# Performance work log

Hardware: AMD Instinct MI355X
Metric: run time of the kernel (lower is better)

The kernel has to match this reference:

```python
import jax, jax.numpy as jnp
import numpy as np

N_NODES = 10000
N_EDGES = 640000
D_IN = 128
D_OUT = 128


def setup_inputs() -> dict:
    key = jax.random.key(0)
    k_x, k_src, k_dst, k_w, k_b = jax.random.split(key, 5)
    x = jax.random.normal(k_x, (N_NODES, D_IN), dtype=jnp.float32)
    src = jax.random.randint(k_src, (N_EDGES,), 0, N_NODES, dtype=jnp.int64)
    dst = jax.random.randint(k_dst, (N_EDGES,), 0, N_NODES, dtype=jnp.int64)
    # nn.Linear default init: U(-1/sqrt(fan_in), 1/sqrt(fan_in))
    bound = 1.0 / np.sqrt(D_IN)
    W = jax.random.uniform(k_w, (D_OUT, D_IN), minval=-bound, maxval=bound, dtype=jnp.float32)
    b = jax.random.uniform(k_b, (D_OUT,), minval=-bound, maxval=bound, dtype=jnp.float32)
    return {"x": x, "src": src, "dst": dst, "W": W, "b": b}


def reference(x, src, dst, W, b):
    # Message passing: gather source-node features per edge, scatter-sum to dst.
    msg = x[src]  # [E, D_IN]
    h = jax.ops.segment_sum(msg, dst, num_segments=N_NODES)  # [N, D_IN]
    # Dense linear: h @ W.T + b
    return jnp.einsum("nd,od->no", h, W) + b
```

## Files before the change

kernel.cpp:

```cpp
#include <hip/hip_runtime.h>
#include <hip/hip_bf16.h>
#include <stdint.h>


#define NBLK 128
#define CBSH 4
#define CBSZ 16
#define NCMAX 640
#define CAP 44
#define CAPN 192

typedef __attribute__((ext_vector_type(8))) short bf16x8;
typedef __attribute__((ext_vector_type(4))) float f32x4;

static __device__ inline unsigned short f2bf(float f) {
    unsigned int u = __float_as_uint(f);
    u += 0x7fffu + ((u >> 16) & 1u);
    return (unsigned short)(u >> 16);
}

__global__ __launch_bounds__(512) void k_fused(const float* __restrict__ x,
                                               const float* __restrict__ W,
                                               unsigned short* __restrict__ y,
                                               int N, int xwb,
                                               const void* __restrict__ srcv,
                                               const void* __restrict__ dstv,
                                               unsigned int* __restrict__ staging,
                                               unsigned short* __restrict__ cnts,
                                               int NC, int E, int C) {
    __shared__ uint4 shbuf[2048];
    __shared__ unsigned int shAny;
    int t = threadIdx.x;
    if ((int)blockIdx.x < NBLK) {
        int* cur = (int*)shbuf;
        if (t == 0) shAny = 0u;
        __syncthreads();
        if (t < 256) {
            unsigned int v = ((const unsigned int*)srcv)[2 * t + 1];
            if (v) atomicOr(&shAny, 1u);
        }
        int bid = blockIdx.x;
        for (int i = t; i < NC; i += 512) cur[i] = (bid * NC + i) * CAP;
        __syncthreads();
        int f64 = shAny ? 0 : 1;
        int beg = bid * C, end = min(E, beg + C);
        int nfull = (end - beg) & ~3;
        if (f64) {
            const long long* s = (const long long*)srcv;
            const long long* d = (const long long*)dstv;
            for (int e0 = beg + 4 * t; e0 < beg + nfull; e0 += 4 * 512) {
                ulonglong2 dA = *(const ulonglong2*)(d + e0);
                ulonglong2 dB = *(const ulonglong2*)(d + e0 + 2);
                ulonglong2 sA = *(const ulonglong2*)(s + e0);
                ulonglong2 sB = *(const ulonglong2*)(s + e0 + 2);
                int dv[4] = {(int)dA.x, (int)dA.y, (int)dB.x, (int)dB.y};
                int sv[4] = {(int)sA.x, (int)sA.y, (int)sB.x, (int)sB.y};
#pragma unroll
                for (int j = 0; j < 4; ++j) {
                    int cb = dv[j] >> CBSH;
                    int pos = atomicAdd(&cur[cb], 1);
                    if (pos - (bid * NC + cb) * CAP < CAP)
                        staging[pos] = ((unsigned int)(dv[j] & (CBSZ - 1)) << 16) |
                                       (unsigned int)sv[j];
                }
            }
            int te = beg + nfull + t;
            if (te < end) {
                int dv = (int)d[te];
                int cb = dv >> CBSH;
                int pos = atomicAdd(&cur[cb], 1);
                if (pos - (bid * NC + cb) * CAP < CAP)
                    staging[pos] = ((unsigned int)(dv & (CBSZ - 1)) << 16) |
                                   (unsigned int)(int)s[te];
            }
        } else {
            const int* s = (const int*)srcv;
            const int* d = (const int*)dstv;
            for (int e0 = beg + 4 * t; e0 < beg + nfull; e0 += 4 * 512) {
                uint4 d4 = *(const uint4*)(d + e0);
                uint4 s4 = *(const uint4*)(s + e0);
                int dv[4] = {(int)d4.x, (int)d4.y, (int)d4.z, (int)d4.w};
                int sv[4] = {(int)s4.x, (int)s4.y, (int)s4.z, (int)s4.w};
#pragma unroll
                for (int j = 0; j < 4; ++j) {
                    int cb = dv[j] >> CBSH;
                    int pos = atomicAdd(&cur[cb], 1);
                    if (pos - (bid * NC + cb) * CAP < CAP)
                        staging[pos] = ((unsigned int)(dv[j] & (CBSZ - 1)) << 16) |
                                       (unsigned int)sv[j];
                }
            }
            int te = beg + nfull + t;
            if (te < end) {
                int dv = d[te];
                int cb = dv >> CBSH;
                int pos = atomicAdd(&cur[cb], 1);
                if (pos - (bid * NC + cb) * CAP < CAP)
                    staging[pos] = ((unsigned int)(dv & (CBSZ - 1)) << 16) |
                                   (unsigned int)s[te];
            }
        }
        __syncthreads();
        for (int i = t; i < NC; i += 512) {
            int cnt = cur[i] - (bid * NC + i) * CAP;
            if (cnt > CAP) cnt = CAP;
            cnts[(size_t)i * NBLK + bid] = (unsigned short)cnt;
        }
    } else {
        for (int i = t; i < 2048; i += 512) {
            int o = i >> 4, g = i & 15;
            const float4* wp = (const float4*)(W + o * 128 + g * 8);
            float4 f0 = wp[0], f1 = wp[1];
            uint4 pk;
            pk.x = (unsigned int)f2bf(f0.x) | ((unsigned int)f2bf(f0.y) << 16);
            pk.y = (unsigned int)f2bf(f0.z) | ((unsigned int)f2bf(f0.w) << 16);
            pk.z = (unsigned int)f2bf(f1.x) | ((unsigned int)f2bf(f1.y) << 16);
            pk.w = (unsigned int)f2bf(f1.z) | ((unsigned int)f2bf(f1.w) << 16);
            shbuf[o * 16 + (g ^ (o & 15))] = pk;
        }
        __syncthreads();
        int wid = (blockIdx.x - NBLK) * 8 + (t >> 6);
        int lane = t & 63;
        int m0 = wid * 16;
        if (m0 >= N) return;
        int r = lane & 15, hi = lane >> 4;
        int mr = m0 + r; if (mr >= N) mr = N - 1;
        bf16x8 a[4];
        const float* xr = x + (size_t)mr * 128 + hi * 8;
#pragma unroll
        for (int kt = 0; kt < 4; ++kt) {
            float4 f0 = *(const float4*)(xr + kt * 32);
            float4 f1 = *(const float4*)(xr + kt * 32 + 4);
            unsigned short* ap = (unsigned short*)&a[kt];
            ap[0]=f2bf(f0.x); ap[1]=f2bf(f0.y); ap[2]=f2bf(f0.z); ap[3]=f2bf(f0.w);
            ap[4]=f2bf(f1.x); ap[5]=f2bf(f1.y); ap[6]=f2bf(f1.z); ap[7]=f2bf(f1.w);
        }
#pragma unroll 2
        for (int ot = 0; ot < 8; ++ot) {
            f32x4 acc = {0.f, 0.f, 0.f, 0.f};
            int o = ot * 16 + r;
#pragma unroll
            for (int kt = 0; kt < 4; ++kt) {
                uint4 wv4 = shbuf[o * 16 + ((kt * 4 + hi) ^ (o & 15))];
                bf16x8 bf;
                *(uint4*)&bf = wv4;
                acc = __builtin_amdgcn_mfma_f32_16x16x32_bf16(a[kt], bf, acc, 0, 0, 0);
            }
#pragma unroll
            for (int reg = 0; reg < 4; ++reg) {
                int m = m0 + hi * 4 + reg;
                if (m < N) y[(size_t)m * 128 + ot * 16 + r] = f2bf(acc[reg]);
            }
        }
    }
}

__global__ __launch_bounds__(512) void k_sortgather(const unsigned int* __restrict__ staging,
                                                    const unsigned short* __restrict__ cnts,
                                                    const unsigned short* __restrict__ y,
                                                    const float* __restrict__ bias,
                                                    float* __restrict__ out,
                                                    int N, int NC) {
    __shared__ unsigned short sorted[CBSZ * CAPN];
    __shared__ int wcnt[NBLK];
    __shared__ int nodeCnt[CBSZ];
    int c = blockIdx.x, t = threadIdx.x;
    if (t < 64) {
        unsigned int pv = ((const unsigned int*)(cnts + (size_t)c * NBLK))[t];
        wcnt[2 * t] = (int)(pv & 0xFFFFu);
        wcnt[2 * t + 1] = (int)(pv >> 16);
    }
    if (t >= 64 && t < 64 + CBSZ) nodeCnt[t - 64] = 0;
    __syncthreads();
    int gq = t >> 3, ln8 = t & 7;
#pragma unroll
    for (int i = 0; i < 2; ++i) {
        int k = gq + i * 64;
        int cw = wcnt[k];
        const unsigned int* srcw = staging + ((size_t)k * NC + c) * CAP;
        for (int j = ln8; j < cw; j += 8) {
            unsigned int p = srcw[j];
            int node = (int)(p >> 16);
            int pos = atomicAdd(&nodeCnt[node], 1);
            if (pos < CAPN)
                sorted[node * CAPN + pos] = (unsigned short)(p & 0xFFFFu);
        }
    }
    __syncthreads();
    int wv = t >> 6, lane = t & 63;
    int r = lane & 15, g = lane >> 4;
    const uint4* yp = (const uint4*)y;
#pragma unroll
    for (int q = 0; q < 2; ++q) {
        int tloc = wv * 2 + q;
        int node = (c << CBSH) + tloc;
        if (node >= N) continue;
        int lcnt = nodeCnt[tloc]; if (lcnt > CAPN) lcnt = CAPN;
        const unsigned short* sl = sorted + tloc * CAPN;
        float2 a0 = {0.f,0.f}, a1 = {0.f,0.f}, a2 = {0.f,0.f}, a3 = {0.f,0.f};
        int nb4 = lcnt >> 2;
#pragma unroll 4
        for (int k = 0; k < nb4; ++k) {
            int sid = (int)sl[4 * k + g];
            uint4 v = yp[(size_t)sid * 16 + r];
            a0.x += __uint_as_float(v.x << 16); a0.y += __uint_as_float(v.x & 0xffff0000u);
            a1.x += __uint_as_float(v.y << 16); a1.y += __uint_as_float(v.y & 0xffff0000u);
            a2.x += __uint_as_float(v.z << 16); a2.y += __uint_as_float(v.z & 0xffff0000u);
            a3.x += __uint_as_float(v.w << 16); a3.y += __uint_as_float(v.w & 0xffff0000u);
        }
        int idx = (nb4 << 2) + g;
        if (idx < lcnt) {
            int sid = (int)sl[idx];
            uint4 v = yp[(size_t)sid * 16 + r];
            a0.x += __uint_as_float(v.x << 16); a0.y += __uint_as_float(v.x & 0xffff0000u);
            a1.x += __uint_as_float(v.y << 16); a1.y += __uint_as_float(v.y & 0xffff0000u);
            a2.x += __uint_as_float(v.z << 16); a2.y += __uint_as_float(v.z & 0xffff0000u);
            a3.x += __uint_as_float(v.w << 16); a3.y += __uint_as_float(v.w & 0xffff0000u);
        }
        a0.x += __shfl_xor(a0.x, 16); a0.x += __shfl_xor(a0.x, 32);
        a0.y += __shfl_xor(a0.y, 16); a0.y += __shfl_xor(a0.y, 32);
        a1.x += __shfl_xor(a1.x, 16); a1.x += __shfl_xor(a1.x, 32);
        a1.y += __shfl_xor(a1.y, 16); a1.y += __shfl_xor(a1.y, 32);
        a2.x += __shfl_xor(a2.x, 16); a2.x += __shfl_xor(a2.x, 32);
        a2.y += __shfl_xor(a2.y, 16); a2.y += __shfl_xor(a2.y, 32);
        a3.x += __shfl_xor(a3.x, 16); a3.x += __shfl_xor(a3.x, 32);
        a3.y += __shfl_xor(a3.y, 16); a3.y += __shfl_xor(a3.y, 32);
        if (lane < 16) {
            float4 b0 = ((const float4*)bias)[r * 2];
            float4 b1 = ((const float4*)bias)[r * 2 + 1];
            float4 o0 = {a0.x + b0.x, a0.y + b0.y, a1.x + b0.z, a1.y + b0.w};
            float4 o1 = {a2.x + b1.x, a2.y + b1.y, a3.x + b1.z, a3.y + b1.w};
            float4* op = (float4*)(out + (size_t)node * 128 + r * 8);
            op[0] = o0;
            op[1] = o1;
        }
    }
}

extern "C" void kernel_launch(void* const* d_in, const int* in_sizes, int n_in,
                              void* d_out, int out_size, void* d_ws, size_t ws_size,
                              hipStream_t stream) {
    const float* x = (const float*)d_in[0];
    const void* srcv = d_in[1];
    const void* dstv = d_in[2];
    const float* W = (const float*)d_in[3];
    const float* bias = (const float*)d_in[4];
    float* out = (float*)d_out;

    const int D = 128;
    int N = in_sizes[0] / D;
    int E = in_sizes[1];
    int C = (E + NBLK - 1) / NBLK;
    int NC = (N + CBSZ - 1) >> CBSH;

    char* ws = (char*)d_ws;
    size_t off = 0;
    auto take = [&](size_t bytes) {
        char* p = ws + off;
        off = (off + bytes + 255) & ~(size_t)255;
        return p;
    };
    unsigned short* y      = (unsigned short*)take((size_t)N * D * 2);
    unsigned int* staging  = (unsigned int*)take((size_t)NBLK * NC * CAP * 4);
    unsigned short* cnts   = (unsigned short*)take((size_t)NC * NBLK * 2);

    int xwb = (((N + 15) / 16) + 7) / 8;

    k_fused<<<NBLK + xwb, 512, 0, stream>>>(x, W, y, N, xwb, srcv, dstv,
                                            staging, cnts, NC, E, C);
    k_sortgather<<<NC, 512, 0, stream>>>(staging, cnts, y, bias, out, N, NC);
}
```

Measured before the change: 29.80 us.

## Double binning blocks and block size, interleave two-node gather loops

Binning now uses 256 blocks of 1024 threads, so each block handles half as many edges, and the per-bucket staging capacity drops from 44 to 24 slots. The GEMM part also runs 1024-thread blocks. In the sort-gather kernel, each wave interleaves the gather loops for its two nodes so more independent loads are in flight, and the count load is widened to four entries per thread. The smaller capacity makes bucket overflow, which silently drops edges, more likely for skewed inputs, and the 1024-thread blocks may reduce occupancy.

```diff
diff --git a/kernel.cpp b/kernel.cpp
--- a/kernel.cpp
+++ b/kernel.cpp
@@ -3,11 +3,11 @@
 #include <stdint.h>
 
 
-#define NBLK 128
+#define NBLK 256
 #define CBSH 4
 #define CBSZ 16
 #define NCMAX 640
-#define CAP 44
+#define CAP 24
 #define CAPN 192
 
 typedef __attribute__((ext_vector_type(8))) short bf16x8;
@@ -19,15 +19,15 @@
     return (unsigned short)(u >> 16);
 }
 
-__global__ __launch_bounds__(512) void k_fused(const float* __restrict__ x,
-                                               const float* __restrict__ W,
-                                               unsigned short* __restrict__ y,
-                                               int N, int xwb,
-                                               const void* __restrict__ srcv,
-                                               const void* __restrict__ dstv,
-                                               unsigned int* __restrict__ staging,
-                                               unsigned short* __restrict__ cnts,
-                                               int NC, int E, int C) {
+__global__ __launch_bounds__(1024) void k_fused(const float* __restrict__ x,
+                                                const float* __restrict__ W,
+                                                unsigned short* __restrict__ y,
+                                                int N, int xwb,
+                                                const void* __restrict__ srcv,
+                                                const void* __restrict__ dstv,
+                                                unsigned int* __restrict__ staging,
+                                                unsigned short* __restrict__ cnts,
+                                                int NC, int E, int C) {
     __shared__ uint4 shbuf[2048];
     __shared__ unsigned int shAny;
     int t = threadIdx.x;
@@ -40,7 +40,7 @@
             if (v) atomicOr(&shAny, 1u);
         }
         int bid = blockIdx.x;
-        for (int i = t; i < NC; i += 512) cur[i] = (bid * NC + i) * CAP;
+        for (int i = t; i < NC; i += 1024) cur[i] = (bid * NC + i) * CAP;
         __syncthreads();
         int f64 = shAny ? 0 : 1;
         int beg = bid * C, end = min(E, beg + C);
@@ -48,7 +48,7 @@
         if (f64) {
             const long long* s = (const long long*)srcv;
             const long long* d = (const long long*)dstv;
-            for (int e0 = beg + 4 * t; e0 < beg + nfull; e0 += 4 * 512) {
+            for (int e0 = beg + 4 * t; e0 < beg + nfull; e0 += 4 * 1024) {
                 ulonglong2 dA = *(const ulonglong2*)(d + e0);
                 ulonglong2 dB = *(const ulonglong2*)(d + e0 + 2);
                 ulonglong2 sA = *(const ulonglong2*)(s + e0);
@@ -76,7 +76,7 @@
         } else {
             const int* s = (const int*)srcv;
             const int* d = (const int*)dstv;
-            for (int e0 = beg + 4 * t; e0 < beg + nfull; e0 += 4 * 512) {
+            for (int e0 = beg + 4 * t; e0 < beg + nfull; e0 += 4 * 1024) {
                 uint4 d4 = *(const uint4*)(d + e0);
                 uint4 s4 = *(const uint4*)(s + e0);
                 int dv[4] = {(int)d4.x, (int)d4.y, (int)d4.z, (int)d4.w};
@@ -101,13 +101,13 @@
             }
         }
         __syncthreads();
-        for (int i = t; i < NC; i += 512) {
+        for (int i = t; i < NC; i += 1024) {
             int cnt = cur[i] - (bid * NC + i) * CAP;
             if (cnt > CAP) cnt = CAP;
             cnts[(size_t)i * NBLK + bid] = (unsigned short)cnt;
         }
     } else {
-        for (int i = t; i < 2048; i += 512) {
+        for (int i = t; i < 2048; i += 1024) {
             int o = i >> 4, g = i & 15;
             const float4* wp = (const float4*)(W + o * 128 + g * 8);
             float4 f0 = wp[0], f1 = wp[1];
@@ -119,7 +119,7 @@
             shbuf[o * 16 + (g ^ (o & 15))] = pk;
         }
         __syncthreads();
-        int wid = (blockIdx.x - NBLK) * 8 + (t >> 6);
+        int wid = (blockIdx.x - NBLK) * 16 + (t >> 6);
         int lane = t & 63;
         int m0 = wid * 16;
         if (m0 >= N) return;
@@ -166,15 +166,17 @@
     __shared__ int nodeCnt[CBSZ];
     int c = blockIdx.x, t = threadIdx.x;
     if (t < 64) {
-        unsigned int pv = ((const unsigned int*)(cnts + (size_t)c * NBLK))[t];
-        wcnt[2 * t] = (int)(pv & 0xFFFFu);
-        wcnt[2 * t + 1] = (int)(pv >> 16);
+        uint2 pv = ((const uint2*)(cnts + (size_t)c * NBLK))[t];
+        wcnt[4*t]   = (int)(pv.x & 0xFFFFu);
+        wcnt[4*t+1] = (int)(pv.x >> 16);
+        wcnt[4*t+2] = (int)(pv.y & 0xFFFFu);
+        wcnt[4*t+3] = (int)(pv.y >> 16);
     }
     if (t >= 64 && t < 64 + CBSZ) nodeCnt[t - 64] = 0;
     __syncthreads();
     int gq = t >> 3, ln8 = t & 7;
 #pragma unroll
-    for (int i = 0; i < 2; ++i) {
+    for (int i = 0; i < 4; ++i) {
         int k = gq + i * 64;
         int cw = wcnt[k];
         const unsigned int* srcw = staging + ((size_t)k * NC + c) * CAP;
@@ -190,49 +192,76 @@
     int wv = t >> 6, lane = t & 63;
     int r = lane & 15, g = lane >> 4;
     const uint4* yp = (const uint4*)y;
-#pragma unroll
-    for (int q = 0; q < 2; ++q) {
-        int tloc = wv * 2 + q;
-        int node = (c << CBSH) + tloc;
-        if (node >= N) continue;
-        int lcnt = nodeCnt[tloc]; if (lcnt > CAPN) lcnt = CAPN;
-        const unsigned short* sl = sorted + tloc * CAPN;
-        float2 a0 = {0.f,0.f}, a1 = {0.f,0.f}, a2 = {0.f,0.f}, a3 = {0.f,0.f};
-        int nb4 = lcnt >> 2;
-#pragma unroll 4
-        for (int k = 0; k < nb4; ++k) {
-            int sid = (int)sl[4 * k + g];
+    int tloc0 = wv * 2, tloc1 = wv * 2 + 1;
+    int node0 = (c << CBSH) + tloc0, node1 = node0 + 1;
+    int lc0 = nodeCnt[tloc0]; if (lc0 > CAPN) lc0 = CAPN;
+    int lc1 = nodeCnt[tloc1]; if (lc1 > CAPN) lc1 = CAPN;
+    const unsigned short* sl0 = sorted + tloc0 * CAPN;
+    const unsigned short* sl1 = sorted + tloc1 * CAPN;
+    float2 p0[4] = {{0.f,0.f},{0.f,0.f},{0.f,0.f},{0.f,0.f}};
+    float2 p1[4] = {{0.f,0.f},{0.f,0.f},{0.f,0.f},{0.f,0.f}};
+    int nb0 = lc0 >> 2, nb1 = lc1 >> 2;
+    int nbmax = nb0 > nb1 ? nb0 : nb1;
+#pragma unroll 2
+    for (int k = 0; k < nbmax; ++k) {
+        if (k < nb0) {
+            int sid = (int)sl0[4 * k + g];
             uint4 v = yp[(size_t)sid * 16 + r];
-            a0.x += __uint_as_float(v.x << 16); a0.y += __uint_as_float(v.x & 0xffff0000u);
-            a1.x += __uint_as_float(v.y << 16); a1.y += __uint_as_float(v.y & 0xffff0000u);
-            a2.x += __uint_as_float(v.z << 16); a2.y += __uint_as_float(v.z & 0xffff0000u);
-            a3.x += __uint_as_float(v.w << 16); a3.y += __uint_as_float(v.w & 0xffff0000u);
-        }
-        int idx = (nb4 << 2) + g;
-        if (idx < lcnt) {
-            int sid = (int)sl[idx];
+            p0[0].x += __uint_as_float(v.x << 16); p0[0].y += __uint_as_float(v.x & 0xffff0000u);
+            p0[1].x += __uint_as_float(v.y << 16); p0[1].y += __uint_as_float(v.y & 0xffff0000u);
+            p0[2].x += __uint_as_float(v.z << 16); p0[2].y += __uint_as_float(v.z & 0xffff0000u);
+            p0[3].x += __uint_as_float(v.w << 16); p0[3].y += __uint_as_float(v.w & 0xffff0000u);
+        }
+        if (k < nb1) {
+            int sid = (int)sl1[4 * k + g];
             uint4 v = yp[(size_t)sid * 16 + r];
-            a0.x += __uint_as_float(v.x << 16); a0.y += __uint_as_float(v.x & 0xffff0000u);
-            a1.x += __uint_as_float(v.y << 16); a1.y += __uint_as_float(v.y & 0xffff0000u);
-            a2.x += __uint_as_float(v.z << 16); a2.y += __uint_as_float(v.z & 0xffff0000u);
-            a3.x += __uint_as_float(v.w << 16); a3.y += __uint_as_float(v.w & 0xffff0000u);
-        }
-        a0.x += __shfl_xor(a0.x, 16); a0.x += __shfl_xor(a0.x, 32);
-        a0.y += __shfl_xor(a0.y, 16); a0.y += __shfl_xor(a0.y, 32);
-        a1.x += __shfl_xor(a1.x, 16); a1.x += __shfl_xor(a1.x, 32);
-        a1.y += __shfl_xor(a1.y, 16); a1.y += __shfl_xor(a1.y, 32);
-        a2.x += __shfl_xor(a2.x, 16); a2.x += __shfl_xor(a2.x, 32);
-        a2.y += __shfl_xor(a2.y, 16); a2.y += __shfl_xor(a2.y, 32);
-        a3.x += __shfl_xor(a3.x, 16); a3.x += __shfl_xor(a3.x, 32);
-        a3.y += __shfl_xor(a3.y, 16); a3.y += __shfl_xor(a3.y, 32);
-        if (lane < 16) {
-            float4 b0 = ((const float4*)bias)[r * 2];
-            float4 b1 = ((const float4*)bias)[r * 2 + 1];
-            float4 o0 = {a0.x + b0.x, a0.y + b0.y, a1.x + b0.z, a1.y + b0.w};
-            float4 o1 = {a2.x + b1.x, a2.y + b1.y, a3.x + b1.z, a3.y + b1.w};
-            float4* op = (float4*)(out + (size_t)node * 128 + r * 8);
-            op[0] = o0;
-            op[1] = o1;
+            p1[0].x += __uint_as_float(v.x << 16); p1[0].y += __uint_as_float(v.x & 0xffff0000u);
+            p1[1].x += __uint_as_float(v.y << 16); p1[1].y += __uint_as_float(v.y & 0xffff0000u);
+            p1[2].x += __uint_as_float(v.z << 16); p1[2].y += __uint_as_float(v.z & 0xffff0000u);
+            p1[3].x += __uint_as_float(v.w << 16); p1[3].y += __uint_as_float(v.w & 0xffff0000u);
+        }
+    }
+    {
+        int idx = (nb0 << 2) + g;
+        if (idx < lc0) {
+            int sid = (int)sl0[idx];
+            uint4 v = yp[(size_t)sid * 16 + r];
+            p0[0].x += __uint_as_float(v.x << 16); p0[0].y += __uint_as_float(v.x & 0xffff0000u);
+            p0[1].x += __uint_as_float(v.y << 16); p0[1].y += __uint_as_float(v.y & 0xffff0000u);
+            p0[2].x += __uint_as_float(v.z << 16); p0[2].y += __uint_as_float(v.z & 0xffff0000u);
+            p0[3].x += __uint_as_float(v.w << 16); p0[3].y += __uint_as_float(v.w & 0xffff0000u);
+        }
+        idx = (nb1 << 2) + g;
+        if (idx < lc1) {
+            int sid = (int)sl1[idx];
+            uint4 v = yp[(size_t)sid * 16 + r];
+            p1[0].x += __uint_as_float(v.x << 16); p1[0].y += __uint_as_float(v.x & 0xffff0000u);
+            p1[1].x += __uint_as_float(v.y << 16); p1[1].y += __uint_as_float(v.y & 0xffff0000u);
+            p1[2].x += __uint_as_float(v.z << 16); p1[2].y += __uint_as_float(v.z & 0xffff0000u);
+            p1[3].x += __uint_as_float(v.w << 16); p1[3].y += __uint_as_float(v.w & 0xffff0000u);
+        }
+    }
+#pragma unroll
+    for (int j = 0; j < 4; ++j) {
+        p0[j].x += __shfl_xor(p0[j].x, 16); p0[j].x += __shfl_xor(p0[j].x, 32);
+        p0[j].y += __shfl_xor(p0[j].y, 16); p0[j].y += __shfl_xor(p0[j].y, 32);
+        p1[j].x += __shfl_xor(p1[j].x, 16); p1[j].x += __shfl_xor(p1[j].x, 32);
+        p1[j].y += __shfl_xor(p1[j].y, 16); p1[j].y += __shfl_xor(p1[j].y, 32);
+    }
+    if (lane < 16) {
+        float4 b0 = ((const float4*)bias)[r * 2];
+        float4 b1 = ((const float4*)bias)[r * 2 + 1];
+        if (node0 < N) {
+            float4 o0 = {p0[0].x + b0.x, p0[0].y + b0.y, p0[1].x + b0.z, p0[1].y + b0.w};
+            float4 o1 = {p0[2].x + b1.x, p0[2].y + b1.y, p0[3].x + b1.z, p0[3].y + b1.w};
+            float4* op = (float4*)(out + (size_t)node0 * 128 + r * 8);
+            op[0] = o0; op[1] = o1;
+        }
+        if (node1 < N) {
+            float4 o0 = {p1[0].x + b0.x, p1[0].y + b0.y, p1[1].x + b0.z, p1[1].y + b0.w};
+            float4 o1 = {p1[2].x + b1.x, p1[2].y + b1.y, p1[3].x + b1.z, p1[3].y + b1.w};
+            float4* op = (float4*)(out + (size_t)node1 * 128 + r * 8);
+            op[0] = o0; op[1] = o1;
         }
     }
 }
@@ -264,9 +293,9 @@
     unsigned int* staging  = (unsigned int*)take((size_t)NBLK * NC * CAP * 4);
     unsigned short* cnts   = (unsigned short*)take((size_t)NC * NBLK * 2);
 
-    int xwb = (((N + 15) / 16) + 7) / 8;
-
-    k_fused<<<NBLK + xwb, 512, 0, stream>>>(x, W, y, N, xwb, srcv, dstv,
-                                            staging, cnts, NC, E, C);
+    int xwb = (((N + 15) / 16) + 15) / 16;
+
+    k_fused<<<NBLK + xwb, 1024, 0, stream>>>(x, W, y, N, xwb, srcv, dstv,
+                                             staging, cnts, NC, E, C);
     k_sortgather<<<NC, 512, 0, stream>>>(staging, cnts, y, bias, out, N, NC);
 }
```

Measured after the change: 38.80 us. +30.2%, slower.

## Merge binning, GEMM and gather into one cooperative kernel with grid sync

Applied to the files above, without the earlier changes.

Adds a cooperative kernel that runs the edge-binning and x·W phases, then a grid-wide barrier, then the per-bin sort and gather loop in a grid-stride loop. The two phases share one shared-memory buffer through a union. The goal is to remove the second kernel launch and the gap between the launches. The cost is a grid barrier and a grid capped at 256 or 512 blocks, so some blocks handle more than one of the 625 bins in the gather phase. The old two-kernel path is kept as a fallback when cooperative launch is not available. Each launch also adds host-side device-property and occupancy queries.

```diff
diff --git a/kernel.cpp b/kernel.cpp
--- a/kernel.cpp
+++ b/kernel.cpp
@@ -1,6 +1,9 @@
 #include <hip/hip_runtime.h>
 #include <hip/hip_bf16.h>
+#include <hip/hip_cooperative_groups.h>
 #include <stdint.h>
+
+namespace cg = cooperative_groups;
 
 
 #define NBLK 128
@@ -13,116 +16,121 @@
 typedef __attribute__((ext_vector_type(8))) short bf16x8;
 typedef __attribute__((ext_vector_type(4))) float f32x4;
 
+struct P2Sh {
+    unsigned short sorted[CBSZ * CAPN];
+    int wcnt[NBLK];
+    int nodeCnt[CBSZ];
+};
+union SharedU {
+    uint4 shbuf[2048];
+    P2Sh p2;
+};
+
 static __device__ inline unsigned short f2bf(float f) {
     unsigned int u = __float_as_uint(f);
     u += 0x7fffu + ((u >> 16) & 1u);
     return (unsigned short)(u >> 16);
 }
 
-__global__ __launch_bounds__(512) void k_fused(const float* __restrict__ x,
-                                               const float* __restrict__ W,
-                                               unsigned short* __restrict__ y,
-                                               int N, int xwb,
-                                               const void* __restrict__ srcv,
-                                               const void* __restrict__ dstv,
-                                               unsigned int* __restrict__ staging,
-                                               unsigned short* __restrict__ cnts,
-                                               int NC, int E, int C) {
-    __shared__ uint4 shbuf[2048];
-    __shared__ unsigned int shAny;
-    int t = threadIdx.x;
-    if ((int)blockIdx.x < NBLK) {
-        int* cur = (int*)shbuf;
-        if (t == 0) shAny = 0u;
-        __syncthreads();
-        if (t < 256) {
-            unsigned int v = ((const unsigned int*)srcv)[2 * t + 1];
-            if (v) atomicOr(&shAny, 1u);
-        }
-        int bid = blockIdx.x;
-        for (int i = t; i < NC; i += 512) cur[i] = (bid * NC + i) * CAP;
-        __syncthreads();
-        int f64 = shAny ? 0 : 1;
-        int beg = bid * C, end = min(E, beg + C);
-        int nfull = (end - beg) & ~3;
-        if (f64) {
-            const long long* s = (const long long*)srcv;
-            const long long* d = (const long long*)dstv;
-            for (int e0 = beg + 4 * t; e0 < beg + nfull; e0 += 4 * 512) {
-                ulonglong2 dA = *(const ulonglong2*)(d + e0);
-                ulonglong2 dB = *(const ulonglong2*)(d + e0 + 2);
-                ulonglong2 sA = *(const ulonglong2*)(s + e0);
-                ulonglong2 sB = *(const ulonglong2*)(s + e0 + 2);
-                int dv[4] = {(int)dA.x, (int)dA.y, (int)dB.x, (int)dB.y};
-                int sv[4] = {(int)sA.x, (int)sA.y, (int)sB.x, (int)sB.y};
-#pragma unroll
-                for (int j = 0; j < 4; ++j) {
-                    int cb = dv[j] >> CBSH;
-                    int pos = atomicAdd(&cur[cb], 1);
-                    if (pos - (bid * NC + cb) * CAP < CAP)
-                        staging[pos] = ((unsigned int)(dv[j] & (CBSZ - 1)) << 16) |
-                                       (unsigned int)sv[j];
-                }
-            }
-            int te = beg + nfull + t;
-            if (te < end) {
-                int dv = (int)d[te];
-                int cb = dv >> CBSH;
+static __device__ __forceinline__ void body_passA(
+        int bid, int t, int* cur, unsigned int* shAny,
+        const void* __restrict__ srcv, const void* __restrict__ dstv,
+        unsigned int* __restrict__ staging, unsigned short* __restrict__ cnts,
+        int NC, int E, int C) {
+    if (t == 0) *shAny = 0u;
+    __syncthreads();
+    if (t < 256) {
+        unsigned int v = ((const unsigned int*)srcv)[2 * t + 1];
+        if (v) atomicOr(shAny, 1u);
+    }
+    for (int i = t; i < NC; i += 512) cur[i] = (bid * NC + i) * CAP;
+    __syncthreads();
+    int f64 = *shAny ? 0 : 1;
+    int beg = bid * C, end = min(E, beg + C);
+    int nfull = (end - beg) & ~3;
+    if (f64) {
+        const long long* s = (const long long*)srcv;
+        const long long* d = (const long long*)dstv;
+        for (int e0 = beg + 4 * t; e0 < beg + nfull; e0 += 4 * 512) {
+            ulonglong2 dA = *(const ulonglong2*)(d + e0);
+            ulonglong2 dB = *(const ulonglong2*)(d + e0 + 2);
+            ulonglong2 sA = *(const ulonglong2*)(s + e0);
+            ulonglong2 sB = *(const ulonglong2*)(s + e0 + 2);
+            int dv[4] = {(int)dA.x, (int)dA.y, (int)dB.x, (int)dB.y};
+            int sv[4] = {(int)sA.x, (int)sA.y, (int)sB.x, (int)sB.y};
+#pragma unroll
+            for (int j = 0; j < 4; ++j) {
+                int cb = dv[j] >> CBSH;
                 int pos = atomicAdd(&cur[cb], 1);
                 if (pos - (bid * NC + cb) * CAP < CAP)
-                    staging[pos] = ((unsigned int)(dv & (CBSZ - 1)) << 16) |
-                                   (unsigned int)(int)s[te];
+                    staging[pos] = ((unsigned int)(dv[j] & (CBSZ - 1)) << 16) |
+                                   (unsigned int)sv[j];
             }
-        } else {
-            const int* s = (const int*)srcv;
-            const int* d = (const int*)dstv;
-            for (int e0 = beg + 4 * t; e0 < beg + nfull; e0 += 4 * 512) {
-                uint4 d4 = *(const uint4*)(d + e0);
-                uint4 s4 = *(const uint4*)(s + e0);
-                int dv[4] = {(int)d4.x, (int)d4.y, (int)d4.z, (int)d4.w};
-                int sv[4] = {(int)s4.x, (int)s4.y, (int)s4.z, (int)s4.w};
-#pragma unroll
-                for (int j = 0; j < 4; ++j) {
-                    int cb = dv[j] >> CBSH;
-                    int pos = atomicAdd(&cur[cb], 1);
-                    if (pos - (bid * NC + cb) * CAP < CAP)
-                        staging[pos] = ((unsigned int)(dv[j] & (CBSZ - 1)) << 16) |
-                                       (unsigned int)sv[j];
-                }
-            }
-            int te = beg + nfull + t;
-            if (te < end) {
-                int dv = d[te];
-                int cb = dv >> CBSH;
+        }
+        int te = beg + nfull + t;
+        if (te < end) {
+            int dv = (int)d[te];
+            int cb = dv >> CBSH;
+            int pos = atomicAdd(&cur[cb], 1);
+            if (pos - (bid * NC + cb) * CAP < CAP)
+                staging[pos] = ((unsigned int)(dv & (CBSZ - 1)) << 16) |
+                               (unsigned int)(int)s[te];
+        }
+    } else {
+        const int* s = (const int*)srcv;
+        const int* d = (const int*)dstv;
+        for (int e0 = beg + 4 * t; e0 < beg + nfull; e0 += 4 * 512) {
+            uint4 d4 = *(const uint4*)(d + e0);
+            uint4 s4 = *(const uint4*)(s + e0);
+            int dv[4] = {(int)d4.x, (int)d4.y, (int)d4.z, (int)d4.w};
+            int sv[4] = {(int)s4.x, (int)s4.y, (int)s4.z, (int)s4.w};
+#pragma unroll
+            for (int j = 0; j < 4; ++j) {
+                int cb = dv[j] >> CBSH;
                 int pos = atomicAdd(&cur[cb], 1);
                 if (pos - (bid * NC + cb) * CAP < CAP)
-                    staging[pos] = ((unsigned int)(dv & (CBSZ - 1)) << 16) |
-                                   (unsigned int)s[te];
+                    staging[pos] = ((unsigned int)(dv[j] & (CBSZ - 1)) << 16) |
+                                   (unsigned int)sv[j];
             }
         }
-        __syncthreads();
-        for (int i = t; i < NC; i += 512) {
-            int cnt = cur[i] - (bid * NC + i) * CAP;
-            if (cnt > CAP) cnt = CAP;
-            cnts[(size_t)i * NBLK + bid] = (unsigned short)cnt;
-        }
-    } else {
-        for (int i = t; i < 2048; i += 512) {
-            int o = i >> 4, g = i & 15;
-            const float4* wp = (const float4*)(W + o * 128 + g * 8);
-            float4 f0 = wp[0], f1 = wp[1];
-            uint4 pk;
-            pk.x = (unsigned int)f2bf(f0.x) | ((unsigned int)f2bf(f0.y) << 16);
-            pk.y = (unsigned int)f2bf(f0.z) | ((unsigned int)f2bf(f0.w) << 16);
-            pk.z = (unsigned int)f2bf(f1.x) | ((unsigned int)f2bf(f1.y) << 16);
-            pk.w = (unsigned int)f2bf(f1.z) | ((unsigned int)f2bf(f1.w) << 16);
-            shbuf[o * 16 + (g ^ (o & 15))] = pk;
-        }
-        __syncthreads();
-        int wid = (blockIdx.x - NBLK) * 8 + (t >> 6);
-        int lane = t & 63;
-        int m0 = wid * 16;
-        if (m0 >= N) return;
+        int te = beg + nfull + t;
+        if (te < end) {
+            int dv = d[te];
+            int cb = dv >> CBSH;
+            int pos = atomicAdd(&cur[cb], 1);
+            if (pos - (bid * NC + cb) * CAP < CAP)
+                staging[pos] = ((unsigned int)(dv & (CBSZ - 1)) << 16) |
+                               (unsigned int)s[te];
+        }
+    }
+    __syncthreads();
+    for (int i = t; i < NC; i += 512) {
+        int cnt = cur[i] - (bid * NC + i) * CAP;
+        if (cnt > CAP) cnt = CAP;
+        cnts[(size_t)i * NBLK + bid] = (unsigned short)cnt;
+    }
+}
+
+static __device__ __forceinline__ void body_xw(
+        int blkoff, int t, uint4* shbuf,
+        const float* __restrict__ x, const float* __restrict__ W,
+        unsigned short* __restrict__ y, int N) {
+    for (int i = t; i < 2048; i += 512) {
+        int o = i >> 4, g = i & 15;
+        const float4* wp = (const float4*)(W + o * 128 + g * 8);
+        float4 f0 = wp[0], f1 = wp[1];
+        uint4 pk;
+        pk.x = (unsigned int)f2bf(f0.x) | ((unsigned int)f2bf(f0.y) << 16);
+        pk.y = (unsigned int)f2bf(f0.z) | ((unsigned int)f2bf(f0.w) << 16);
+        pk.z = (unsigned int)f2bf(f1.x) | ((unsigned int)f2bf(f1.y) << 16);
+        pk.w = (unsigned int)f2bf(f1.z) | ((unsigned int)f2bf(f1.w) << 16);
+        shbuf[o * 16 + (g ^ (o & 15))] = pk;
+    }
+    __syncthreads();
+    int wid = blkoff * 8 + (t >> 6);
+    int lane = t & 63;
+    int m0 = wid * 16;
+    if (m0 < N) {
         int r = lane & 15, hi = lane >> 4;
         int mr = m0 + r; if (mr >= N) mr = N - 1;
         bf16x8 a[4];
@@ -155,35 +163,32 @@
     }
 }
 
-__global__ __launch_bounds__(512) void k_sortgather(const unsigned int* __restrict__ staging,
-                                                    const unsigned short* __restrict__ cnts,
-                                                    const unsigned short* __restrict__ y,
-                                                    const float* __restrict__ bias,
-                                                    float* __restrict__ out,
-                                                    int N, int NC) {
-    __shared__ unsigned short sorted[CBSZ * CAPN];
-    __shared__ int wcnt[NBLK];
-    __shared__ int nodeCnt[CBSZ];
-    int c = blockIdx.x, t = threadIdx.x;
+static __device__ __forceinline__ void body_bin(
+        int c, int t, P2Sh* sh,
+        const unsigned int* __restrict__ staging,
+        const unsigned short* __restrict__ cnts,
+        const unsigned short* __restrict__ y,
+        const float* __restrict__ bias, float* __restrict__ out,
+        int N, int NC) {
     if (t < 64) {
         unsigned int pv = ((const unsigned int*)(cnts + (size_t)c * NBLK))[t];
-        wcnt[2 * t] = (int)(pv & 0xFFFFu);
-        wcnt[2 * t + 1] = (int)(pv >> 16);
-    }
-    if (t >= 64 && t < 64 + CBSZ) nodeCnt[t - 64] = 0;
+        sh->wcnt[2 * t] = (int)(pv & 0xFFFFu);
+        sh->wcnt[2 * t + 1] = (int)(pv >> 16);
+    }
+    if (t >= 64 && t < 64 + CBSZ) sh->nodeCnt[t - 64] = 0;
     __syncthreads();
     int gq = t >> 3, ln8 = t & 7;
 #pragma unroll
     for (int i = 0; i < 2; ++i) {
         int k = gq + i * 64;
-        int cw = wcnt[k];
+        int cw = sh->wcnt[k];
         const unsigned int* srcw = staging + ((size_t)k * NC + c) * CAP;
         for (int j = ln8; j < cw; j += 8) {
             unsigned int p = srcw[j];
             int node = (int)(p >> 16);
-            int pos = atomicAdd(&nodeCnt[node], 1);
+            int pos = atomicAdd(&sh->nodeCnt[node], 1);
             if (pos < CAPN)
-                sorted[node * CAPN + pos] = (unsigned short)(p & 0xFFFFu);
+                sh->sorted[node * CAPN + pos] = (unsigned short)(p & 0xFFFFu);
         }
     }
     __syncthreads();
@@ -195,8 +200,8 @@
         int tloc = wv * 2 + q;
         int node = (c << CBSH) + tloc;
         if (node >= N) continue;
-        int lcnt = nodeCnt[tloc]; if (lcnt > CAPN) lcnt = CAPN;
-        const unsigned short* sl = sorted + tloc * CAPN;
+        int lcnt = sh->nodeCnt[tloc]; if (lcnt > CAPN) lcnt = CAPN;
+        const unsigned short* sl = sh->sorted + tloc * CAPN;
         float2 a0 = {0.f,0.f}, a1 = {0.f,0.f}, a2 = {0.f,0.f}, a3 = {0.f,0.f};
         int nb4 = lcnt >> 2;
 #pragma unroll 4
@@ -237,6 +242,58 @@
     }
 }
 
+__global__ __launch_bounds__(512) void k_fused(const float* __restrict__ x,
+                                               const float* __restrict__ W,
+                                               unsigned short* __restrict__ y,
+                                               int N, int xwb,
+                                               const void* __restrict__ srcv,
+                                               const void* __restrict__ dstv,
+                                               unsigned int* __restrict__ staging,
+                                               unsigned short* __restrict__ cnts,
+                                               int NC, int E, int C) {
+    __shared__ uint4 shbuf[2048];
+    __shared__ unsigned int shAny;
+    if ((int)blockIdx.x < NBLK)
+        body_passA(blockIdx.x, threadIdx.x, (int*)shbuf, &shAny,
+                   srcv, dstv, staging, cnts, NC, E, C);
+    else
+        body_xw(blockIdx.x - NBLK, threadIdx.x, shbuf, x, W, y, N);
+}
+
+__global__ __launch_bounds__(512) void k_sortgather(const unsigned int* __restrict__ staging,
+                                                    const unsigned short* __restrict__ cnts,
+                                                    const unsigned short* __restrict__ y,
+                                                    const float* __restrict__ bias,
+                                                    float* __restrict__ out,
+                                                    int N, int NC) {
+    __shared__ P2Sh sh2;
+    body_bin(blockIdx.x, threadIdx.x, &sh2, staging, cnts, y, bias, out, N, NC);
+}
+
+__global__ __launch_bounds__(512) void k_all(
+        const float* __restrict__ x, const float* __restrict__ W,
+        unsigned short* __restrict__ y, int N, int xwb,
+        const void* __restrict__ srcv, const void* __restrict__ dstv,
+        unsigned int* __restrict__ staging, unsigned short* __restrict__ cnts,
+        int NC, int E, int C,
+        const float* __restrict__ bias, float* __restrict__ out) {
+    __shared__ SharedU sh;
+    __shared__ unsigned int shAny;
+    int t = threadIdx.x;
+    if ((int)blockIdx.x < NBLK)
+        body_passA(blockIdx.x, t, (int*)sh.shbuf, &shAny,
+                   srcv, dstv, staging, cnts, NC, E, C);
+    else if ((int)blockIdx.x < NBLK + xwb)
+        body_xw(blockIdx.x - NBLK, t, sh.shbuf, x, W, y, N);
+
+    cg::this_grid().sync();
+
+    for (int c = blockIdx.x; c < NC; c += gridDim.x) {
+        __syncthreads();
+        body_bin(c, t, &sh.p2, staging, cnts, y, bias, out, N, NC);
+    }
+}
+
 extern "C" void kernel_launch(void* const* d_in, const int* in_sizes, int n_in,
                               void* d_out, int out_size, void* d_ws, size_t ws_size,
                               hipStream_t stream) {
@@ -266,7 +323,23 @@
 
     int xwb = (((N + 15) / 16) + 7) / 8;
 
-    k_fused<<<NBLK + xwb, 512, 0, stream>>>(x, W, y, N, xwb, srcv, dstv,
-                                            staging, cnts, NC, E, C);
-    k_sortgather<<<NC, 512, 0, stream>>>(staging, cnts, y, bias, out, N, NC);
-}
+    int dev = 0;
+    hipGetDevice(&dev);
+    hipDeviceProp_t prop;
+    hipGetDeviceProperties(&prop, dev);
+    int maxPerCU = 0;
+    hipOccupancyMaxActiveBlocksPerMultiprocessor(&maxPerCU, k_all, 512, 0);
+    long long maxCoop = (long long)maxPerCU * prop.multiProcessorCount;
+    int GRIDB = (maxCoop >= 512) ? 512 : 256;
+
+    if (prop.cooperativeLaunch && maxCoop >= GRIDB && GRIDB >= NBLK + xwb) {
+        void* args[] = {&x, &W, &y, &N, &xwb, &srcv, &dstv, &staging, &cnts,
+                        &NC, &E, &C, &bias, &out};
+        hipLaunchCooperativeKernel((void*)k_all, dim3(GRIDB), dim3(512),
+                                   args, 0, stream);
+    } else {
+        k_fused<<<NBLK + xwb, 512, 0, stream>>>(x, W, y, N, xwb, srcv, dstv,
+                                                staging, cnts, NC, E, C);
+        k_sortgather<<<NC, 512, 0, stream>>>(staging, cnts, y, bias, out, N, NC);
+    }
+}
```

New measurement: 84.47 us. 2.83x slower.
